# Kernel tuning notes

Hardware: AMD Instinct MI355X
Metric: run time of the kernel (lower is better)

Reference implementation:

```python
import jax, jax.numpy as jnp
from jax import lax
import numpy as np

B, CIN, COUT, H, W = 8, 64, 64, 128, 128
K = 3
KK = K * K  # 9 kernel taps


def setup_inputs() -> dict:
    key = jax.random.key(0)
    ks = jax.random.split(key, 10)
    n = jax.random.normal
    s = 0.05  # keep activations in a sane range
    return {
        "Fi": n(ks[0], (B, CIN, H, W), jnp.float32),
        "Fe": n(ks[1], (B, CIN, H, W), jnp.float32),
        "w1": n(ks[2], (CIN, 2 * CIN, 5, 5), jnp.float32) * s,
        "b1": n(ks[3], (CIN,), jnp.float32) * s,
        "w2": n(ks[4], (CIN, CIN, 3, 3), jnp.float32) * s,
        "b2": n(ks[5], (CIN,), jnp.float32) * s,
        "w_off": n(ks[6], (3 * KK, CIN, 3, 3), jnp.float32) * s,
        "b_off": n(ks[7], (3 * KK,), jnp.float32) * s,
        "w_dcn": n(ks[8], (COUT, CIN, 3, 3), jnp.float32) * s,
        "b_dcn": n(ks[9], (COUT,), jnp.float32) * s,
    }


def _conv(x, w, b, pad):
    y = lax.conv_general_dilated(x, w, (1, 1), [(pad, pad), (pad, pad)],
                                 dimension_numbers=('NCHW', 'OIHW', 'NCHW'))
    return y + b[None, :, None, None]


def _leaky(x):
    return jnp.where(x >= 0, x, 0.1 * x)  # LeakyReLU(0.1)


def _bilinear(img, y, x):
    # img [B,C,H,W]; y, x [B,KK,H,W] fractional sampling coords; zero padding OOB
    Bn, C, Hi, Wi = img.shape
    y0 = jnp.floor(y)
    x0 = jnp.floor(x)
    flat = img.reshape(Bn, C, Hi * Wi)
    out = jnp.zeros((Bn, C) + y.shape[1:], img.dtype)
    for dy, dx in ((0, 0), (0, 1), (1, 0), (1, 1)):
        yi = y0 + dy
        xi = x0 + dx
        wgt = (1.0 - jnp.abs(y - yi)) * (1.0 - jnp.abs(x - xi))
        valid = (yi >= 0) & (yi <= Hi - 1) & (xi >= 0) & (xi <= Wi - 1)
        yc = jnp.clip(yi, 0, Hi - 1).astype(jnp.int32)
        xc = jnp.clip(xi, 0, Wi - 1).astype(jnp.int32)
        idx = (yc * Wi + xc).reshape(Bn, 1, -1)
        v = jnp.take_along_axis(flat, jnp.broadcast_to(idx, (Bn, C, idx.shape[-1])), axis=2)
        v = v.reshape(Bn, C, *y.shape[1:])  # [B,C,KK,H,W]
        out = out + v * (wgt * valid)[:, None]
    return out


def _dcn(x, feat, w_off, b_off, w, b):
    # modulated deformable conv (DCNv2), k=3, stride=1, pad=1, dilation=1
    oo = _conv(feat, w_off, b_off, 1)                 # [B, 3*KK, H, W]
    o1, o2, m = jnp.split(oo, 3, axis=1)              # dy, dx, mask logits
    offset_out = jnp.concatenate([o1, o2], axis=1)
    mask = jax.nn.sigmoid(m)                          # [B,KK,H,W]
    ky, kx = jnp.meshgrid(jnp.arange(K), jnp.arange(K), indexing='ij')
    ky = ky.reshape(KK)
    kx = kx.reshape(KK)
    base_y = (jnp.arange(H)[None, :, None] - 1 + ky[:, None, None]).astype(x.dtype)  # [KK,H,1]
    base_x = (jnp.arange(W)[None, None, :] - 1 + kx[:, None, None]).astype(x.dtype)  # [KK,1,W]
    ys = base_y[None] + o1                            # [B,KK,H,W]
    xs = base_x[None] + o2                            # [B,KK,H,W]
    samp = _bilinear(x, ys, xs) * mask[:, None]       # [B,C,KK,H,W]
    out = jnp.einsum('bckhw,ock->bohw', samp, w.reshape(w.shape[0], w.shape[1], KK))
    return offset_out, out + b[None, :, None, None]


def reference(Fi, Fe, w1, b1, w2, b2, w_off, b_off, w_dcn, b_dcn):
    feat = _leaky(_conv(jnp.concatenate([Fi, Fe], axis=1), w1, b1, 2))
    feat = _leaky(_conv(feat, w2, b2, 1))
    offset_out, aligned = _dcn(Fe, feat, w_off, b_off, w_dcn, b_dcn)
    Ff = jnp.concatenate([Fi, aligned], axis=1)
    return offset_out, Ff
```

## Files before the change

kernel.cpp:

```cpp
#include <hip/hip_runtime.h>
#include <hip/hip_bf16.h>

typedef __bf16 bf16_t;
typedef __attribute__((ext_vector_type(8))) __bf16 bf16x8;
typedef __attribute__((ext_vector_type(4))) float f32x4;

#define Bn 8
#define Hh 128
#define Ww 128
#define HW 16384

#define WP1_B   ((size_t)0)
#define WP2_B   ((size_t)409600)
#define WPO_B   ((size_t)483328)
#define WDCN_B  ((size_t)520192)
#define BIAS_B  ((size_t)667648)
#define XT_B    ((size_t)668672)
#define F1_B    (XT_B + 33554432)
#define F2_B    (F1_B + 16777216)

__global__ void prep_kernel(const float* __restrict__ w1, const float* __restrict__ w2,
                            const float* __restrict__ woff, const float* __restrict__ wdcn,
                            const float* __restrict__ b1, const float* __restrict__ b2,
                            const float* __restrict__ boff, const float* __restrict__ bdcn,
                            char* __restrict__ wsb) {
    bf16_t* wp1 = (bf16_t*)(wsb + WP1_B);
    bf16_t* wp2 = (bf16_t*)(wsb + WP2_B);
    bf16_t* wpo = (bf16_t*)(wsb + WPO_B);
    bf16_t* wd  = (bf16_t*)(wsb + WDCN_B);
    float*  bias= (float*)(wsb + BIAS_B);
    int tid = blockIdx.x * blockDim.x + threadIdx.x;
    int nt  = gridDim.x * blockDim.x;
    for (int i = tid; i < 25*4*4*64*8; i += nt) {
        int j = i & 7, q = i >> 3;
        int n = q % 64; q /= 64;
        int g = q & 3;  q >>= 2;
        int ck = q & 3; int t = q >> 2;
        int cin = ck*32 + g*8 + j;
        wp1[i] = (bf16_t)w1[(n*128 + cin)*25 + t];
    }
    for (int i = tid; i < 9*2*4*64*8; i += nt) {
        int j = i & 7, q = i >> 3;
        int n = q % 64; q /= 64;
        int g = q & 3;  q >>= 2;
        int ck = q & 1; int t = q >> 1;
        int cin = ck*32 + g*8 + j;
        wp2[i] = (bf16_t)w2[(n*64 + cin)*9 + t];
    }
    for (int i = tid; i < 9*2*4*32*8; i += nt) {
        int j = i & 7, q = i >> 3;
        int n = q & 31; q >>= 5;
        int g = q & 3;  q >>= 2;
        int ck = q & 1; int t = q >> 1;
        int cin = ck*32 + g*8 + j;
        wpo[i] = (n < 27) ? (bf16_t)woff[(n*64 + cin)*9 + t] : (bf16_t)0.f;
    }
    for (int i = tid; i < 18*4*4*16*8; i += nt) {
        int j = i & 7, f = i >> 3;
        int l15 = f & 15; f >>= 4;
        int l4  = f & 3;  f >>= 2;
        int ntl = f & 3;  int kc = f >> 2;
        int kg = kc*32 + l4*8 + j;
        int tap = kg >> 6, c = kg & 63;
        int n = ntl*16 + l15;
        wd[i] = (bf16_t)wdcn[n*576 + c*9 + tap];
    }
    if (tid < 64) { bias[tid] = b1[tid]; bias[64+tid] = b2[tid]; bias[160+tid] = bdcn[tid]; }
    if (tid >= 64 && tid < 96) { int n = tid - 64; bias[128+n] = (n < 27) ? boff[n] : 0.f; }
}

__global__ __launch_bounds__(256) void nhwc_kernel(const float* __restrict__ Fi,
                                                   const float* __restrict__ Fe,
                                                   bf16_t* __restrict__ Xt) {
    __shared__ bf16_t tile[64][136];
    const int b  = blockIdx.y;
    const int p0 = blockIdx.x * 64;
    const int px = threadIdx.x & 63;
    const int csub = threadIdx.x >> 6;
    for (int ci = 0; ci < 32; ++ci) {
        int c = csub * 32 + ci;
        const float* src = (c < 64) ? (Fi + (((size_t)(b*64 + c)) << 14))
                                    : (Fe + (((size_t)(b*64 + (c-64))) << 14));
        tile[px][c] = (bf16_t)src[p0 + px];
    }
    __syncthreads();
    const int px2 = threadIdx.x >> 2;
    const int cc  = (threadIdx.x & 3) * 32;
    bf16x8* dst = (bf16x8*)(Xt + ((size_t)(b*HW) + p0 + px2) * 128 + cc);
    const bf16x8* srcl = (const bf16x8*)(&tile[px2][cc]);
    dst[0] = srcl[0]; dst[1] = srcl[1]; dst[2] = srcl[2]; dst[3] = srcl[3];
}

template <int CIN_, int KS, int COUTP, bool LEAKY, bool OUTF32, bool OFFS>
__global__ __launch_bounds__(256) void conv_mfma(const bf16_t* __restrict__ Xt,
                                                 const bf16_t* __restrict__ Wp,
                                                 const float* __restrict__ bias,
                                                 bf16_t* __restrict__ outb,
                                                 float* __restrict__ outf,
                                                 float* __restrict__ out0) {
    constexpr int PAD = KS / 2;
    constexpr int HR  = 4 + KS - 1;
    constexpr int HC  = 64 + KS - 1;
    constexpr int NC  = CIN_ / 32;
    constexpr int NT  = COUTP / 16;
    __shared__ bf16_t stg[HR * HC * 40];

    const int tid  = threadIdx.x;
    const int lane = tid & 63;
    const int wid  = tid >> 6;
    const int b    = blockIdx.z;
    const int h0   = blockIdx.y * 4;
    const int w0   = blockIdx.x * 64;
    const int l15  = lane & 15;
    const int l4   = lane >> 4;

    f32x4 acc[4][NT];
#pragma unroll
    for (int m = 0; m < 4; ++m)
#pragma unroll
        for (int nt = 0; nt < NT; ++nt)
#pragma unroll
            for (int r = 0; r < 4; ++r) acc[m][nt][r] = 0.f;

    const bf16_t Z0 = (bf16_t)0.f;
    const bf16x8 zv = {Z0, Z0, Z0, Z0, Z0, Z0, Z0, Z0};
    const bf16x8* wpt = (const bf16x8*)Wp;

    for (int ck = 0; ck < NC; ++ck) {
        for (int s = tid; s < HR * HC; s += 256) {
            const int srow = s / HC, scol = s % HC;
            const int gh = h0 - PAD + srow, gw = w0 - PAD + scol;
            bf16x8 v0 = zv, v1 = zv, v2 = zv, v3 = zv;
            if (((unsigned)gh < 128u) && ((unsigned)gw < 128u)) {
                const bf16x8* gp = (const bf16x8*)(Xt + (((size_t)(b*HW) + (gh << 7) + gw)) * CIN_ + ck * 32);
                v0 = gp[0]; v1 = gp[1]; v2 = gp[2]; v3 = gp[3];
            }
            bf16x8* ldst = (bf16x8*)(&stg[s * 40]);
            ldst[0] = v0; ldst[1] = v1; ldst[2] = v2; ldst[3] = v3;
        }
        __syncthreads();
        int t = 0;
#pragma unroll
        for (int dy = 0; dy < KS; ++dy) {
#pragma unroll
            for (int dx = 0; dx < KS; ++dx, ++t) {
                bf16x8 a[4];
#pragma unroll
                for (int m = 0; m < 4; ++m)
                    a[m] = *(const bf16x8*)(&stg[((wid + dy) * HC + (m * 16 + l15 + dx)) * 40 + l4 * 8]);
                bf16x8 bb[NT];
#pragma unroll
                for (int nt = 0; nt < NT; ++nt)
                    bb[nt] = wpt[((size_t)((t * NC + ck) * 4 + l4)) * COUTP + nt * 16 + l15];
#pragma unroll
                for (int m = 0; m < 4; ++m)
#pragma unroll
                    for (int nt = 0; nt < NT; ++nt)
                        acc[m][nt] = __builtin_amdgcn_mfma_f32_16x16x32_bf16(a[m], bb[nt], acc[m][nt], 0, 0, 0);
            }
        }
        __syncthreads();
    }

    const int hrow = h0 + wid;
#pragma unroll
    for (int m = 0; m < 4; ++m) {
#pragma unroll
        for (int nt = 0; nt < NT; ++nt) {
            const int n = nt * 16 + l15;
            const float bs = bias[n];
#pragma unroll
            for (int r = 0; r < 4; ++r) {
                const int px = w0 + m * 16 + l4 * 4 + r;
                float v = acc[m][nt][r] + bs;
                if (LEAKY) v = (v >= 0.f) ? v : 0.1f * v;
                const size_t pix = (size_t)(hrow << 7) + px;
                if (OUTF32) outf[(((size_t)(b * COUTP + n)) << 14) + pix] = v;
                else        outb[(((size_t)(b * HW)) + pix) * COUTP + n] = (bf16_t)v;
                if (OFFS) {
                    if (n < 18) out0[(((size_t)(b * 18 + n)) << 14) + pix] = v;
                }
            }
        }
    }
}

__global__ void copy_fi(const float* __restrict__ Fi, float* __restrict__ out1) {
    const int b = blockIdx.y;
    const int i = blockIdx.x * blockDim.x + threadIdx.x;
    const int e = i << 2;
    const int c = e >> 14;
    const int p = e & 16383;
    const float4* src = reinterpret_cast<const float4*>(Fi);
    float4* dst = reinterpret_cast<float4*>(out1);
    size_t se = ((size_t)b << 20) + e;
    size_t de = (((size_t)(b * 128 + c)) << 14) + p;
    dst[de >> 2] = src[se >> 2];
}

__global__ __launch_bounds__(256, 4) void dcn_mfma(const bf16_t* __restrict__ Xt,
                                                   const float* __restrict__ OO,
                                                   const bf16_t* __restrict__ Wd,
                                                   const float* __restrict__ bias,
                                                   float* __restrict__ out1) {
    const int tid  = threadIdx.x;
    const int lane = tid & 63;
    const int wave = tid >> 6;
    const int l15  = lane & 15;
    const int l4   = lane >> 4;
    const int b    = blockIdx.y;
    const int p0   = blockIdx.x * 64 + wave * 16;

    f32x4 acc[4];
#pragma unroll
    for (int nt = 0; nt < 4; ++nt) {
        const float bs = bias[nt * 16 + l15];
        acc[nt][0] = bs; acc[nt][1] = bs; acc[nt][2] = bs; acc[nt][3] = bs;
    }

    const bf16_t* feb = Xt + ((size_t)(b * HW)) * 128 + 64;
    const bf16x8* Wdv = (const bf16x8*)Wd;

    const int p = p0 + l15;
    const int h = p >> 7, w = p & 127;
    const size_t oobase = (((size_t)(b * 32)) << 14) + p;

#pragma unroll
    for (int k = 0; k < 9; ++k) {
        const int ky = k / 3, kx = k % 3;
        const float o1v = OO[oobase + ((size_t)k << 14)];
        const float o2v = OO[oobase + ((size_t)(9 + k) << 14)];
        const float ml  = OO[oobase + ((size_t)(18 + k) << 14)];
        const float m = 1.f / (1.f + __expf(-ml));

        const float y = (float)(h - 1 + ky) + o1v;
        const float x = (float)(w - 1 + kx) + o2v;
        const float y0f = floorf(y), x0f = floorf(x);
        const float fy = y - y0f, fx = x - x0f;
        const int y0 = (int)y0f, x0 = (int)x0f;

        const bool vy0 = (unsigned)y0 < 128u;
        const bool vy1 = (unsigned)(y0 + 1) < 128u;
        const bool vx0 = (unsigned)x0 < 128u;
        const bool vx1 = (unsigned)(x0 + 1) < 128u;

        const int y0c = min(max(y0, 0), 127);
        const int y1c = min(max(y0 + 1, 0), 127);
        const int x0c = min(max(x0, 0), 127);
        const int x1c = min(max(x0 + 1, 0), 127);

        float w00 = (1.f - fy) * (1.f - fx) * m; w00 = (vy0 && vx0) ? w00 : 0.f;
        float w01 = (1.f - fy) * fx * m;         w01 = (vy0 && vx1) ? w01 : 0.f;
        float w10 = fy * (1.f - fx) * m;         w10 = (vy1 && vx0) ? w10 : 0.f;
        float w11 = fy * fx * m;                 w11 = (vy1 && vx1) ? w11 : 0.f;

        const bf16_t* p00 = feb + ((size_t)((y0c << 7) + x0c)) * 128;
        const bf16_t* p01 = feb + ((size_t)((y0c << 7) + x1c)) * 128;
        const bf16_t* p10 = feb + ((size_t)((y1c << 7) + x0c)) * 128;
        const bf16_t* p11 = feb + ((size_t)((y1c << 7) + x1c)) * 128;

#pragma unroll
        for (int cc = 0; cc < 2; ++cc) {
            const int c0 = cc * 32 + l4 * 8;
            const bf16x8 v00 = *(const bf16x8*)(p00 + c0);
            const bf16x8 v01 = *(const bf16x8*)(p01 + c0);
            const bf16x8 v10 = *(const bf16x8*)(p10 + c0);
            const bf16x8 v11 = *(const bf16x8*)(p11 + c0);
            bf16x8 af;
#pragma unroll
            for (int j = 0; j < 8; ++j) {
                af[j] = (bf16_t)(w00 * (float)v00[j] + w01 * (float)v01[j]
                               + w10 * (float)v10[j] + w11 * (float)v11[j]);
            }
            const int kc = k * 2 + cc;
#pragma unroll
            for (int nt = 0; nt < 4; ++nt) {
                const bf16x8 bf = Wdv[((kc * 4 + nt) * 4 + l4) * 16 + l15];
                acc[nt] = __builtin_amdgcn_mfma_f32_16x16x32_bf16(af, bf, acc[nt], 0, 0, 0);
            }
        }
    }

#pragma unroll
    for (int nt = 0; nt < 4; ++nt) {
        const int o = nt * 16 + l15;
#pragma unroll
        for (int r = 0; r < 4; ++r) {
            const int px = p0 + l4 * 4 + r;
            out1[(((size_t)(b * 128 + 64 + o)) << 14) + px] = acc[nt][r];
        }
    }
}

extern "C" void kernel_launch(void* const* d_in, const int* in_sizes, int n_in,
                              void* d_out, int out_size, void* d_ws, size_t ws_size,
                              hipStream_t stream) {
    const float* Fi    = (const float*)d_in[0];
    const float* Fe    = (const float*)d_in[1];
    const float* w1    = (const float*)d_in[2];
    const float* b1    = (const float*)d_in[3];
    const float* w2    = (const float*)d_in[4];
    const float* b2    = (const float*)d_in[5];
    const float* w_off = (const float*)d_in[6];
    const float* b_off = (const float*)d_in[7];
    const float* w_dcn = (const float*)d_in[8];
    const float* b_dcn = (const float*)d_in[9];

    char* wsb = (char*)d_ws;
    bf16_t* wp1   = (bf16_t*)(wsb + WP1_B);
    bf16_t* wp2   = (bf16_t*)(wsb + WP2_B);
    bf16_t* wpo   = (bf16_t*)(wsb + WPO_B);
    bf16_t* wdcnf = (bf16_t*)(wsb + WDCN_B);
    float*  bias  = (float*)(wsb + BIAS_B);
    bf16_t* Xt    = (bf16_t*)(wsb + XT_B);
    bf16_t* feat1 = (bf16_t*)(wsb + F1_B);
    bf16_t* feat2 = (bf16_t*)(wsb + F2_B);
    float*  OO    = (float*)(wsb + F1_B);

    float* out0 = (float*)d_out;
    float* out1 = out0 + (size_t)Bn * 18 * HW;

    prep_kernel<<<256, 256, 0, stream>>>(w1, w2, w_off, w_dcn, b1, b2, b_off, b_dcn, wsb);

    nhwc_kernel<<<dim3(256, 8), 256, 0, stream>>>(Fi, Fe, Xt);

    conv_mfma<128, 5, 64, true, false, false>
        <<<dim3(2, 32, 8), 256, 0, stream>>>(Xt, wp1, bias, feat1, nullptr, nullptr);

    conv_mfma<64, 3, 64, true, false, false>
        <<<dim3(2, 32, 8), 256, 0, stream>>>(feat1, wp2, bias + 64, feat2, nullptr, nullptr);

    conv_mfma<64, 3, 32, false, true, true>
        <<<dim3(2, 32, 8), 256, 0, stream>>>(feat2, wpo, bias + 128, nullptr, OO, out0);

    copy_fi<<<dim3(1024, 8), 256, 0, stream>>>(Fi, out1);

    dcn_mfma<<<dim3(256, 8), 256, 0, stream>>>(Xt, OO, wdcnf, bias + 160, out1);
}
```

Before: 336.3 us.

## Software-pipeline DCN bilinear gathers and interleave batches across blocks

Rewrites the deformable-conv kernel's main loop as an 18-stage software pipeline with double-buffered gather registers. The loads for the next channel-half or tap are issued before the current stage's blend and MFMAs, which is meant to hide gather latency. Offset, mask and sigmoid values are precomputed for all 9 taps up front. The grid becomes 1D with batch as the fastest-varying index, which changes how blocks are ordered across the GPU. The cost is higher register pressure, which may reduce occupancy under the 256x4 launch bound.

```diff
diff --git a/kernel.cpp b/kernel.cpp
--- a/kernel.cpp
+++ b/kernel.cpp
@@ -208,8 +208,9 @@
     const int wave = tid >> 6;
     const int l15  = lane & 15;
     const int l4   = lane >> 4;
-    const int b    = blockIdx.y;
-    const int p0   = blockIdx.x * 64 + wave * 16;
+    const int blk  = blockIdx.x;
+    const int b    = blk & 7;
+    const int p0   = (blk >> 3) * 64 + wave * 16;
 
     f32x4 acc[4];
 #pragma unroll
@@ -224,62 +225,89 @@
     const int p = p0 + l15;
     const int h = p >> 7, w = p & 127;
     const size_t oobase = (((size_t)(b * 32)) << 14) + p;
-
+    const int c0 = l4 * 8;
+    const int c1 = 32 + l4 * 8;
+
+    float ys[9], xs[9], ms[9];
 #pragma unroll
     for (int k = 0; k < 9; ++k) {
-        const int ky = k / 3, kx = k % 3;
         const float o1v = OO[oobase + ((size_t)k << 14)];
         const float o2v = OO[oobase + ((size_t)(9 + k) << 14)];
-        const float ml  = OO[oobase + ((size_t)(18 + k) << 14)];
-        const float m = 1.f / (1.f + __expf(-ml));
-
-        const float y = (float)(h - 1 + ky) + o1v;
-        const float x = (float)(w - 1 + kx) + o2v;
-        const float y0f = floorf(y), x0f = floorf(x);
-        const float fy = y - y0f, fx = x - x0f;
-        const int y0 = (int)y0f, x0 = (int)x0f;
-
-        const bool vy0 = (unsigned)y0 < 128u;
-        const bool vy1 = (unsigned)(y0 + 1) < 128u;
-        const bool vx0 = (unsigned)x0 < 128u;
-        const bool vx1 = (unsigned)(x0 + 1) < 128u;
-
-        const int y0c = min(max(y0, 0), 127);
-        const int y1c = min(max(y0 + 1, 0), 127);
-        const int x0c = min(max(x0, 0), 127);
-        const int x1c = min(max(x0 + 1, 0), 127);
-
-        float w00 = (1.f - fy) * (1.f - fx) * m; w00 = (vy0 && vx0) ? w00 : 0.f;
-        float w01 = (1.f - fy) * fx * m;         w01 = (vy0 && vx1) ? w01 : 0.f;
-        float w10 = fy * (1.f - fx) * m;         w10 = (vy1 && vx0) ? w10 : 0.f;
-        float w11 = fy * fx * m;                 w11 = (vy1 && vx1) ? w11 : 0.f;
-
-        const bf16_t* p00 = feb + ((size_t)((y0c << 7) + x0c)) * 128;
-        const bf16_t* p01 = feb + ((size_t)((y0c << 7) + x1c)) * 128;
-        const bf16_t* p10 = feb + ((size_t)((y1c << 7) + x0c)) * 128;
-        const bf16_t* p11 = feb + ((size_t)((y1c << 7) + x1c)) * 128;
-
-#pragma unroll
-        for (int cc = 0; cc < 2; ++cc) {
-            const int c0 = cc * 32 + l4 * 8;
-            const bf16x8 v00 = *(const bf16x8*)(p00 + c0);
-            const bf16x8 v01 = *(const bf16x8*)(p01 + c0);
-            const bf16x8 v10 = *(const bf16x8*)(p10 + c0);
-            const bf16x8 v11 = *(const bf16x8*)(p11 + c0);
-            bf16x8 af;
-#pragma unroll
-            for (int j = 0; j < 8; ++j) {
-                af[j] = (bf16_t)(w00 * (float)v00[j] + w01 * (float)v01[j]
-                               + w10 * (float)v10[j] + w11 * (float)v11[j]);
-            }
-            const int kc = k * 2 + cc;
-#pragma unroll
-            for (int nt = 0; nt < 4; ++nt) {
-                const bf16x8 bf = Wdv[((kc * 4 + nt) * 4 + l4) * 16 + l15];
-                acc[nt] = __builtin_amdgcn_mfma_f32_16x16x32_bf16(af, bf, acc[nt], 0, 0, 0);
-            }
-        }
-    }
+        const float mlv = OO[oobase + ((size_t)(18 + k) << 14)];
+        ys[k] = (float)(h - 1 + (k / 3)) + o1v;
+        xs[k] = (float)(w - 1 + (k % 3)) + o2v;
+        ms[k] = 1.f / (1.f + __expf(-mlv));
+    }
+
+    bf16x8 g[2][4];
+    float  wq[2][4];
+    int    toff[4];
+
+#define DCN_ISSUE_EVEN(k)                                                        \
+    do {                                                                         \
+        const float yk = ys[(k)], xk = xs[(k)];                                  \
+        const float y0f = floorf(yk), x0f = floorf(xk);                          \
+        const float fy = yk - y0f, fx = xk - x0f;                                \
+        const int y0 = (int)y0f, x0 = (int)x0f;                                  \
+        const bool vy0 = (unsigned)y0 < 128u;                                    \
+        const bool vy1 = (unsigned)(y0 + 1) < 128u;                              \
+        const bool vx0 = (unsigned)x0 < 128u;                                    \
+        const bool vx1 = (unsigned)(x0 + 1) < 128u;                              \
+        const int y0c = min(max(y0, 0), 127), y1c = min(max(y0 + 1, 0), 127);    \
+        const int x0c = min(max(x0, 0), 127), x1c = min(max(x0 + 1, 0), 127);    \
+        const float mk = ms[(k)];                                                \
+        float a00 = (1.f - fy) * (1.f - fx) * mk; a00 = (vy0 && vx0) ? a00 : 0.f;\
+        float a01 = (1.f - fy) * fx * mk;         a01 = (vy0 && vx1) ? a01 : 0.f;\
+        float a10 = fy * (1.f - fx) * mk;         a10 = (vy1 && vx0) ? a10 : 0.f;\
+        float a11 = fy * fx * mk;                 a11 = (vy1 && vx1) ? a11 : 0.f;\
+        wq[0][0] = a00; wq[0][1] = a01; wq[0][2] = a10; wq[0][3] = a11;          \
+        toff[0] = (y0c << 7) + x0c; toff[1] = (y0c << 7) + x1c;                  \
+        toff[2] = (y1c << 7) + x0c; toff[3] = (y1c << 7) + x1c;                  \
+        g[0][0] = *(const bf16x8*)(feb + (((size_t)toff[0]) << 7) + c0);         \
+        g[0][1] = *(const bf16x8*)(feb + (((size_t)toff[1]) << 7) + c0);         \
+        g[0][2] = *(const bf16x8*)(feb + (((size_t)toff[2]) << 7) + c0);         \
+        g[0][3] = *(const bf16x8*)(feb + (((size_t)toff[3]) << 7) + c0);         \
+    } while (0)
+
+#define DCN_ISSUE_ODD()                                                          \
+    do {                                                                         \
+        wq[1][0] = wq[0][0]; wq[1][1] = wq[0][1];                                \
+        wq[1][2] = wq[0][2]; wq[1][3] = wq[0][3];                                \
+        g[1][0] = *(const bf16x8*)(feb + (((size_t)toff[0]) << 7) + c1);         \
+        g[1][1] = *(const bf16x8*)(feb + (((size_t)toff[1]) << 7) + c1);         \
+        g[1][2] = *(const bf16x8*)(feb + (((size_t)toff[2]) << 7) + c1);         \
+        g[1][3] = *(const bf16x8*)(feb + (((size_t)toff[3]) << 7) + c1);         \
+    } while (0)
+
+#define DCN_CONSUME(s)                                                           \
+    do {                                                                         \
+        bf16x8 af;                                                               \
+        _Pragma("unroll")                                                        \
+        for (int j = 0; j < 8; ++j)                                              \
+            af[j] = (bf16_t)(wq[(s) & 1][0] * (float)g[(s) & 1][0][j]            \
+                           + wq[(s) & 1][1] * (float)g[(s) & 1][1][j]            \
+                           + wq[(s) & 1][2] * (float)g[(s) & 1][2][j]            \
+                           + wq[(s) & 1][3] * (float)g[(s) & 1][3][j]);          \
+        _Pragma("unroll")                                                        \
+        for (int nt = 0; nt < 4; ++nt) {                                         \
+            const bf16x8 bfr = Wdv[(((s) * 4 + nt) * 4 + l4) * 16 + l15];        \
+            acc[nt] = __builtin_amdgcn_mfma_f32_16x16x32_bf16(af, bfr, acc[nt], 0, 0, 0); \
+        }                                                                        \
+    } while (0)
+
+    DCN_ISSUE_EVEN(0);
+#pragma unroll
+    for (int s = 0; s < 18; ++s) {
+        if (s + 1 < 18) {
+            if ((s + 1) & 1) DCN_ISSUE_ODD();
+            else             DCN_ISSUE_EVEN((s + 1) >> 1);
+        }
+        DCN_CONSUME(s);
+    }
+
+#undef DCN_ISSUE_EVEN
+#undef DCN_ISSUE_ODD
+#undef DCN_CONSUME
 
 #pragma unroll
     for (int nt = 0; nt < 4; ++nt) {
@@ -335,5 +363,5 @@
 
     copy_fi<<<dim3(1024, 8), 256, 0, stream>>>(Fi, out1);
 
-    dcn_mfma<<<dim3(256, 8), 256, 0, stream>>>(Xt, OO, wdcnf, bias + 160, out1);
-}
+    dcn_mfma<<<2048, 256, 0, stream>>>(Xt, OO, wdcnf, bias + 160, out1);
+}
```

New measurement: 334.3 us. No clear change (-0.6%).

## Stage DCN input tiles in LDS and fuse Fi copy into NHWC transpose

Applied to the files above, without the earlier changes.

The deformable conv kernel now works on 8x8 spatial tiles. Each block preloads a 14x14 halo region of Fe channels into swizzled shared memory, and bilinear samples that land inside the region are served from LDS instead of scattered global loads, with a global fallback for the rest. Offsets and masks are loaded up front. The separate copy_fi kernel is removed and the Fi passthrough is written inside the NHWC conversion kernel, which saves one launch and a second read of Fi. The costs are extra LDS use and a block-level sync, and the Fi stores in the transpose kernel are scalar rather than float4.

```diff
diff --git a/kernel.cpp b/kernel.cpp
--- a/kernel.cpp
+++ b/kernel.cpp
@@ -71,7 +71,8 @@
 
 __global__ __launch_bounds__(256) void nhwc_kernel(const float* __restrict__ Fi,
                                                    const float* __restrict__ Fe,
-                                                   bf16_t* __restrict__ Xt) {
+                                                   bf16_t* __restrict__ Xt,
+                                                   float* __restrict__ out1) {
     __shared__ bf16_t tile[64][136];
     const int b  = blockIdx.y;
     const int p0 = blockIdx.x * 64;
@@ -81,7 +82,9 @@
         int c = csub * 32 + ci;
         const float* src = (c < 64) ? (Fi + (((size_t)(b*64 + c)) << 14))
                                     : (Fe + (((size_t)(b*64 + (c-64))) << 14));
-        tile[px][c] = (bf16_t)src[p0 + px];
+        const float v = src[p0 + px];
+        tile[px][c] = (bf16_t)v;
+        if (c < 64) out1[(((size_t)(b*128 + c)) << 14) + p0 + px] = v;
     }
     __syncthreads();
     const int px2 = threadIdx.x >> 2;
@@ -185,31 +188,37 @@
     }
 }
 
-__global__ void copy_fi(const float* __restrict__ Fi, float* __restrict__ out1) {
-    const int b = blockIdx.y;
-    const int i = blockIdx.x * blockDim.x + threadIdx.x;
-    const int e = i << 2;
-    const int c = e >> 14;
-    const int p = e & 16383;
-    const float4* src = reinterpret_cast<const float4*>(Fi);
-    float4* dst = reinterpret_cast<float4*>(out1);
-    size_t se = ((size_t)b << 20) + e;
-    size_t de = (((size_t)(b * 128 + c)) << 14) + p;
-    dst[de >> 2] = src[se >> 2];
-}
-
 __global__ __launch_bounds__(256, 4) void dcn_mfma(const bf16_t* __restrict__ Xt,
                                                    const float* __restrict__ OO,
                                                    const bf16_t* __restrict__ Wd,
                                                    const float* __restrict__ bias,
                                                    float* __restrict__ out1) {
+    __shared__ bf16_t fe[196 * 64];
+
     const int tid  = threadIdx.x;
     const int lane = tid & 63;
     const int wave = tid >> 6;
     const int l15  = lane & 15;
     const int l4   = lane >> 4;
-    const int b    = blockIdx.y;
-    const int p0   = blockIdx.x * 64 + wave * 16;
+    const int blk  = blockIdx.x;
+    const int b    = blk & 7;
+    const int tile = blk >> 3;
+    const int h0   = (tile >> 4) << 3;
+    const int w0   = (tile & 15) << 3;
+    const int r0   = h0 - 3, c0 = w0 - 3;
+
+    const bf16_t Z0 = (bf16_t)0.f;
+    const bf16x8 zv = {Z0, Z0, Z0, Z0, Z0, Z0, Z0, Z0};
+
+    for (int i = tid; i < 196 * 8; i += 256) {
+        const int pos = i >> 3, slot = i & 7;
+        const int rr = pos / 14, cq = pos % 14;
+        const int gh = r0 + rr, gw = c0 + cq;
+        bf16x8 v = zv;
+        if (((unsigned)gh < 128u) && ((unsigned)gw < 128u))
+            v = *(const bf16x8*)(Xt + (((size_t)(b * HW) + (gh << 7) + gw)) * 128 + 64 + slot * 8);
+        *(bf16x8*)(&fe[pos * 64 + ((slot * 8) ^ ((pos & 7) << 3))]) = v;
+    }
 
     f32x4 acc[4];
 #pragma unroll
@@ -218,25 +227,31 @@
         acc[nt][0] = bs; acc[nt][1] = bs; acc[nt][2] = bs; acc[nt][3] = bs;
     }
 
+    const int prow = h0 + (wave << 1) + (l15 >> 3);
+    const int pcol = w0 + (l15 & 7);
+    const size_t oobase = (((size_t)(b * 32)) << 14) + (prow << 7) + pcol;
+
+    float ys[9], xs[9], ms[9];
+#pragma unroll
+    for (int k = 0; k < 9; ++k) {
+        const float o1v = OO[oobase + ((size_t)k << 14)];
+        const float o2v = OO[oobase + ((size_t)(9 + k) << 14)];
+        const float mlv = OO[oobase + ((size_t)(18 + k) << 14)];
+        ys[k] = (float)(prow - 1 + (k / 3)) + o1v;
+        xs[k] = (float)(pcol - 1 + (k % 3)) + o2v;
+        ms[k] = 1.f / (1.f + __expf(-mlv));
+    }
+
     const bf16_t* feb = Xt + ((size_t)(b * HW)) * 128 + 64;
     const bf16x8* Wdv = (const bf16x8*)Wd;
 
-    const int p = p0 + l15;
-    const int h = p >> 7, w = p & 127;
-    const size_t oobase = (((size_t)(b * 32)) << 14) + p;
+    __syncthreads();
 
 #pragma unroll
     for (int k = 0; k < 9; ++k) {
-        const int ky = k / 3, kx = k % 3;
-        const float o1v = OO[oobase + ((size_t)k << 14)];
-        const float o2v = OO[oobase + ((size_t)(9 + k) << 14)];
-        const float ml  = OO[oobase + ((size_t)(18 + k) << 14)];
-        const float m = 1.f / (1.f + __expf(-ml));
-
-        const float y = (float)(h - 1 + ky) + o1v;
-        const float x = (float)(w - 1 + kx) + o2v;
-        const float y0f = floorf(y), x0f = floorf(x);
-        const float fy = y - y0f, fx = x - x0f;
+        const float yk = ys[k], xk = xs[k];
+        const float y0f = floorf(yk), x0f = floorf(xk);
+        const float fy = yk - y0f, fx = xk - x0f;
         const int y0 = (int)y0f, x0 = (int)x0f;
 
         const bool vy0 = (unsigned)y0 < 128u;
@@ -244,39 +259,46 @@
         const bool vx0 = (unsigned)x0 < 128u;
         const bool vx1 = (unsigned)(x0 + 1) < 128u;
 
-        const int y0c = min(max(y0, 0), 127);
-        const int y1c = min(max(y0 + 1, 0), 127);
-        const int x0c = min(max(x0, 0), 127);
-        const int x1c = min(max(x0 + 1, 0), 127);
-
-        float w00 = (1.f - fy) * (1.f - fx) * m; w00 = (vy0 && vx0) ? w00 : 0.f;
-        float w01 = (1.f - fy) * fx * m;         w01 = (vy0 && vx1) ? w01 : 0.f;
-        float w10 = fy * (1.f - fx) * m;         w10 = (vy1 && vx0) ? w10 : 0.f;
-        float w11 = fy * fx * m;                 w11 = (vy1 && vx1) ? w11 : 0.f;
-
-        const bf16_t* p00 = feb + ((size_t)((y0c << 7) + x0c)) * 128;
-        const bf16_t* p01 = feb + ((size_t)((y0c << 7) + x1c)) * 128;
-        const bf16_t* p10 = feb + ((size_t)((y1c << 7) + x0c)) * 128;
-        const bf16_t* p11 = feb + ((size_t)((y1c << 7) + x1c)) * 128;
+        const float mk = ms[k];
+        float w00 = (1.f - fy) * (1.f - fx) * mk; w00 = (vy0 && vx0) ? w00 : 0.f;
+        float w01 = (1.f - fy) * fx * mk;         w01 = (vy0 && vx1) ? w01 : 0.f;
+        float w10 = fy * (1.f - fx) * mk;         w10 = (vy1 && vx0) ? w10 : 0.f;
+        float w11 = fy * fx * mk;                 w11 = (vy1 && vx1) ? w11 : 0.f;
+
+        const int ry = y0 - r0, rx = x0 - c0;
+        const bool inreg = ((unsigned)ry < 13u) && ((unsigned)rx < 13u);
+        const int pos00 = ry * 14 + rx;
 
 #pragma unroll
         for (int cc = 0; cc < 2; ++cc) {
-            const int c0 = cc * 32 + l4 * 8;
-            const bf16x8 v00 = *(const bf16x8*)(p00 + c0);
-            const bf16x8 v01 = *(const bf16x8*)(p01 + c0);
-            const bf16x8 v10 = *(const bf16x8*)(p10 + c0);
-            const bf16x8 v11 = *(const bf16x8*)(p11 + c0);
+            const int slot = cc * 4 + l4;
+            bf16x8 v00, v01, v10, v11;
+            if (inreg) {
+                const int sw = slot * 8;
+                v00 = *(const bf16x8*)(&fe[(pos00     ) * 64 + (sw ^ (((pos00     ) & 7) << 3))]);
+                v01 = *(const bf16x8*)(&fe[(pos00 +  1) * 64 + (sw ^ (((pos00 +  1) & 7) << 3))]);
+                v10 = *(const bf16x8*)(&fe[(pos00 + 14) * 64 + (sw ^ (((pos00 + 14) & 7) << 3))]);
+                v11 = *(const bf16x8*)(&fe[(pos00 + 15) * 64 + (sw ^ (((pos00 + 15) & 7) << 3))]);
+            } else {
+                const int y0c = min(max(y0, 0), 127), y1c = min(max(y0 + 1, 0), 127);
+                const int x0c = min(max(x0, 0), 127), x1c = min(max(x0 + 1, 0), 127);
+                const int ch = slot * 8;
+                v00 = *(const bf16x8*)(feb + ((size_t)((y0c << 7) + x0c)) * 128 + ch);
+                v01 = *(const bf16x8*)(feb + ((size_t)((y0c << 7) + x1c)) * 128 + ch);
+                v10 = *(const bf16x8*)(feb + ((size_t)((y1c << 7) + x0c)) * 128 + ch);
+                v11 = *(const bf16x8*)(feb + ((size_t)((y1c << 7) + x1c)) * 128 + ch);
+            }
             bf16x8 af;
 #pragma unroll
             for (int j = 0; j < 8; ++j) {
                 af[j] = (bf16_t)(w00 * (float)v00[j] + w01 * (float)v01[j]
                                + w10 * (float)v10[j] + w11 * (float)v11[j]);
             }
-            const int kc = k * 2 + cc;
+            const int s = k * 2 + cc;
 #pragma unroll
             for (int nt = 0; nt < 4; ++nt) {
-                const bf16x8 bf = Wdv[((kc * 4 + nt) * 4 + l4) * 16 + l15];
-                acc[nt] = __builtin_amdgcn_mfma_f32_16x16x32_bf16(af, bf, acc[nt], 0, 0, 0);
+                const bf16x8 bfr = Wdv[((s * 4 + nt) * 4 + l4) * 16 + l15];
+                acc[nt] = __builtin_amdgcn_mfma_f32_16x16x32_bf16(af, bfr, acc[nt], 0, 0, 0);
             }
         }
     }
@@ -286,8 +308,10 @@
         const int o = nt * 16 + l15;
 #pragma unroll
         for (int r = 0; r < 4; ++r) {
-            const int px = p0 + l4 * 4 + r;
-            out1[(((size_t)(b * 128 + 64 + o)) << 14) + px] = acc[nt][r];
+            const int i = l4 * 4 + r;
+            const int orow = h0 + (wave << 1) + (i >> 3);
+            const int ocol = w0 + (i & 7);
+            out1[(((size_t)(b * 128 + 64 + o)) << 14) + (orow << 7) + ocol] = acc[nt][r];
         }
     }
 }
@@ -322,7 +346,7 @@
 
     prep_kernel<<<256, 256, 0, stream>>>(w1, w2, w_off, w_dcn, b1, b2, b_off, b_dcn, wsb);
 
-    nhwc_kernel<<<dim3(256, 8), 256, 0, stream>>>(Fi, Fe, Xt);
+    nhwc_kernel<<<dim3(256, 8), 256, 0, stream>>>(Fi, Fe, Xt, out1);
 
     conv_mfma<128, 5, 64, true, false, false>
         <<<dim3(2, 32, 8), 256, 0, stream>>>(Xt, wp1, bias, feat1, nullptr, nullptr);
@@ -333,7 +357,5 @@
     conv_mfma<64, 3, 32, false, true, true>
         <<<dim3(2, 32, 8), 256, 0, stream>>>(feat2, wpo, bias + 128, nullptr, OO, out0);
 
-    copy_fi<<<dim3(1024, 8), 256, 0, stream>>>(Fi, out1);
-
-    dcn_mfma<<<dim3(256, 8), 256, 0, stream>>>(Xt, OO, wdcnf, bias + 160, out1);
-}
+    dcn_mfma<<<2048, 256, 0, stream>>>(Xt, OO, wdcnf, bias + 160, out1);
+}
```

After: 305.9 us. -9.0%, faster.
